# Optimization experiments

Hardware: AMD Instinct MI355X
Metric: run time of the kernel (lower is better)

Reference implementation:

```python
import jax, jax.numpy as jnp
import numpy as np

EPS_NORM = 1e-4
EPS_LOG = 1e-6


def normed_weight(W):
    # W: [O, I, K] (K=1). normalize() over dims (1,2) per output channel,
    # with norm scaled by alpha = sqrt(O / (O*I*K)) = 1/sqrt(I*K), then
    # divided again by sqrt(I*K) in get_normed_weight (eval path).
    O, I, K = W.shape
    fan_in = I * K
    norm = jnp.sqrt(jnp.sum(jnp.square(W), axis=(1, 2), keepdims=True))  # [O,1,1]
    norm = EPS_NORM + norm / np.sqrt(fan_in)
    return (W / norm) / np.sqrt(fan_in)


def complex_log(x):
    real = jnp.log(jnp.maximum(jnp.abs(x), EPS_LOG))
    imag = jnp.where(x < 0, jnp.pi, 0.0).astype(real.dtype)
    return jax.lax.complex(real, imag)


def logcumsumexp_complex(z, axis=-1):
    # stable complex logcumsumexp via associative scan:
    # logaddexp(a, b) = m + log(exp(a-m) + exp(b-m)), m = max(Re a, Re b)
    def combine(a, b):
        m = jnp.maximum(a.real, b.real)
        mc = jax.lax.complex(m, jnp.zeros_like(m))
        return mc + jnp.log(jnp.exp(a - mc) + jnp.exp(b - mc))
    return jax.lax.associative_scan(combine, z, axis=axis)


def min_gru(h, g):
    # h, g: [B, C, L]; parallel log-space minGRU recurrence along L
    log_scale = 0.5 * jnp.log(1.0 / jnp.cosh(g) + 1.0)
    log_coeffs = -jax.nn.softplus(g) + log_scale                 # real
    log_values = (-jax.nn.softplus(-g) + log_scale) + complex_log(h)  # complex
    a_star = jnp.cumsum(log_coeffs, axis=-1)                     # real
    a_star_c = jax.lax.complex(a_star, jnp.zeros_like(a_star))
    log_h = a_star_c + logcumsumexp_complex(log_values - a_star_c, axis=-1)
    return jnp.exp(log_h).real


def scaled_cat(xs, axis):
    Ns = [x.shape[axis] for x in xs]
    scale = np.sqrt(np.mean(Ns))
    return scale * jnp.concatenate([x * n ** -0.5 for n, x in zip(Ns, xs)], axis=axis)


def setup_inputs() -> dict:
    key = jax.random.key(0)
    k1, k2 = jax.random.split(key)
    B, D, L = 8, 512, 8192
    x = jax.random.normal(k1, (B, D, L), dtype=jnp.float32)
    W = jax.random.normal(k2, (2 * D, D, 1), dtype=jnp.float32)  # Conv1d(dim, 2*dim, 1) weight
    return {"x": x, "W": W}


def reference(x, W):
    Wn = normed_weight(W)  # [2D, D, 1]
    fb = jnp.einsum('oi,bil->bol', Wn[:, :, 0], x)  # [B, 2D, L]
    fore, back = jnp.split(fb, 2, axis=1)
    h_f, g_f = jnp.split(fore, 2, axis=1)
    back_r = back[..., ::-1]
    h_b, g_b = jnp.split(back_r, 2, axis=1)
    out_f = min_gru(h_f, g_f)
    out_b = min_gru(h_b, g_b)[..., ::-1]
    return scaled_cat([out_f, out_b], axis=1)
```

## Files before the change

### kernel.cpp

```cpp
#include <hip/hip_runtime.h>
#include <math.h>
#include <stdint.h>

#define LSEQ 8192
#define DIN  512
#define NB   8
#define NO   1024

typedef __bf16 bf16x8 __attribute__((ext_vector_type(8)));
typedef float f32x16 __attribute__((ext_vector_type(16)));

__device__ __forceinline__ uint32_t pack_bf16_rne(float lo, float hi) {
    uint32_t ul = __builtin_bit_cast(uint32_t, lo);
    uint32_t uh = __builtin_bit_cast(uint32_t, hi);
    ul += 0x7FFFu + ((ul >> 16) & 1u);
    uh += 0x7FFFu + ((uh >> 16) & 1u);
    return (ul >> 16) | (uh & 0xFFFF0000u);
}
__device__ __forceinline__ float bf16_lo(uint32_t w) {
    return __builtin_bit_cast(float, w << 16);
}
__device__ __forceinline__ float bf16_hi(uint32_t w) {
    return __builtin_bit_cast(float, w & 0xFFFF0000u);
}

__device__ __forceinline__ void gl_lds16(const void* g, void* l) {
    __builtin_amdgcn_global_load_lds(
        (const __attribute__((address_space(1))) void*)g,
        (__attribute__((address_space(3))) void*)l, 16, 0, 0);
}


__global__ void norm_kernel(const float* __restrict__ W, uint32_t* __restrict__ Wnb) {
    const int o = blockIdx.x;
    const int lane = threadIdx.x;
    const float* row = W + (size_t)o * DIN;
    float4 v0 = *(const float4*)(row + lane * 4);
    float4 v1 = *(const float4*)(row + 256 + lane * 4);
    float s = v0.x * v0.x + v0.y * v0.y + v0.z * v0.z + v0.w * v0.w
            + v1.x * v1.x + v1.y * v1.y + v1.z * v1.z + v1.w * v1.w;
#pragma unroll
    for (int m = 32; m; m >>= 1) s += __shfl_xor(s, m, 64);
    const float sq = 22.62741699796952f;
    const float scale = 1.0f / ((1e-4f + sqrtf(s) / sq) * sq);
    uint2 w0, w1;
    w0.x = pack_bf16_rne(v0.x * scale, v0.y * scale);
    w0.y = pack_bf16_rne(v0.z * scale, v0.w * scale);
    w1.x = pack_bf16_rne(v1.x * scale, v1.y * scale);
    w1.y = pack_bf16_rne(v1.z * scale, v1.w * scale);
    const int ot = o >> 7, mb = (o >> 5) & 3, m31 = o & 31;
    const int it0 = lane >> 3;
    const int q   = (lane >> 1) & 3;
    const int wic = (lane & 1) * 2;
    uint32_t* base = Wnb + (size_t)ot * 32768 + ((mb * 4 + q) * 32 + m31) * 4 + wic;
    *(uint2*)&base[(size_t)it0 * 2048] = w0;
    *(uint2*)&base[(size_t)(it0 + 8) * 2048] = w1;
}

__global__ __launch_bounds__(256)
void xpack_kernel(const float* __restrict__ x, uint32_t* __restrict__ xp) {
    __shared__ uint32_t sT[32 * 132];
    const int t  = threadIdx.x;
    const int bx = blockIdx.x;
    const int b  = blockIdx.y;
    const int lt = bx >> 3;
    const int ch = bx & 7;

    const float* xb = x + (size_t)b * DIN * LSEQ + lt * 128;
#pragma unroll
    for (int j = 0; j < 4; ++j) {
        const int idx = j * 256 + t;
        const int k2l = idx >> 5;
        const int lg  = idx & 31;
        const float* r0 = xb + (size_t)(2 * (ch * 32 + k2l)) * LSEQ + lg * 4;
        float4 a = *(const float4*)r0;
        float4 c = *(const float4*)(r0 + LSEQ);
        uint4 wv;
        wv.x = pack_bf16_rne(a.x, c.x);
        wv.y = pack_bf16_rne(a.y, c.y);
        wv.z = pack_bf16_rne(a.z, c.z);
        wv.w = pack_bf16_rne(a.w, c.w);
        *(uint4*)&sT[k2l * 132 + lg * 4] = wv;
    }
    __syncthreads();
    uint32_t* ob = xp + (size_t)(b * 64 + lt) * 32768;
#pragma unroll
    for (int j = 0; j < 4; ++j) {
        const int idx = j * 256 + t;
        const int lp  = idx >> 3;
        const int gq  = idx & 7;
        uint4 wv;
        wv.x = sT[(gq * 4 + 0) * 132 + lp];
        wv.y = sT[(gq * 4 + 1) * 132 + lp];
        wv.z = sT[(gq * 4 + 2) * 132 + lp];
        wv.w = sT[(gq * 4 + 3) * 132 + lp];
        const int itl   = ch * 2 + (gq >> 2);
        const int q     = gq & 3;
        const int chunk = ((lp >> 5) * 4 + q) * 32 + (lp & 31);
        *(uint4*)&ob[(size_t)itl * 2048 + chunk * 4] = wv;
    }
}

__global__ __launch_bounds__(256)
void gemm_kernel(const uint32_t* __restrict__ Wnb, const uint32_t* __restrict__ xp,
                 uint32_t* __restrict__ fbp) {
    __shared__ uint32_t sA[2][2048];
    __shared__ uint32_t sB[2][2048];

    const int tid  = threadIdx.x;
    const int lane = tid & 63;
    const int w    = tid >> 6;
    const int wm   = w & 1, wn = w >> 1;

    const int bx  = blockIdx.x;
    const int xcd = bx & 7;
    const int t   = bx >> 3;
    const int o0t = t & 7;
    const int o0  = o0t * 128;
    const int ltg = xcd + ((t >> 3) << 3);
    const int l0  = ltg * 128;
    const int b   = blockIdx.y;

    const uint32_t* gA = Wnb + (size_t)o0t * 32768 + (w * 2) * 256 + lane * 4;
    const uint32_t* gB = xp + (size_t)(b * 64 + ltg) * 32768 + (w * 2) * 256 + lane * 4;

    f32x16 acc[2][2];
#pragma unroll
    for (int i = 0; i < 2; ++i)
#pragma unroll
        for (int j = 0; j < 2; ++j)
#pragma unroll
            for (int r = 0; r < 16; ++r) acc[i][j][r] = 0.f;

#define STAGE(it, bs)                                               \
    do {                                                            \
        gl_lds16(gA + (size_t)(it) * 2048, &sA[bs][w * 512]);       \
        gl_lds16(gA + (size_t)(it) * 2048 + 256, &sA[bs][w * 512 + 256]); \
        gl_lds16(gB + (size_t)(it) * 2048, &sB[bs][w * 512]);       \
        gl_lds16(gB + (size_t)(it) * 2048 + 256, &sB[bs][w * 512 + 256]); \
    } while (0)

    STAGE(0, 0);
#pragma unroll 2
    for (int it = 0; it < 16; ++it) {
        const int cb = it & 1;
        __syncthreads();
        if (it + 1 < 16) STAGE(it + 1, cb ^ 1);
        const uint32_t* cA = sA[cb];
        const uint32_t* cB = sB[cb];
#pragma unroll
        for (int kh = 0; kh < 2; ++kh) {
            bf16x8 af[2], bfr[2];
#pragma unroll
            for (int ms = 0; ms < 2; ++ms)
                af[ms] = *(const bf16x8*)&cA[((wm * 2 + ms) * 4 + kh * 2) * 128 + lane * 4];
#pragma unroll
            for (int ns = 0; ns < 2; ++ns)
                bfr[ns] = *(const bf16x8*)&cB[((wn * 2 + ns) * 4 + kh * 2) * 128 + lane * 4];
#pragma unroll
            for (int ms = 0; ms < 2; ++ms)
#pragma unroll
                for (int ns = 0; ns < 2; ++ns)
                    acc[ms][ns] = __builtin_amdgcn_mfma_f32_32x32x16_bf16(
                        af[ms], bfr[ns], acc[ms][ns], 0, 0, 0);
        }
    }
#undef STAGE

    uint32_t* fbp_b = fbp + (size_t)b * 512 * LSEQ + l0;
#pragma unroll
    for (int ms = 0; ms < 2; ++ms)
#pragma unroll
        for (int ns = 0; ns < 2; ++ns) {
            const f32x16 a = acc[ms][ns];
            const int rb = o0 + wm * 64 + ms * 32 + 4 * (lane >> 5);
            const int cc = wn * 64 + ns * 32 + (lane & 31);
#pragma unroll
            for (int rp = 0; rp < 8; ++rp) {
                const int r = rp * 2;
                const int row = rb + (r & 3) + 8 * (r >> 2);
                fbp_b[(size_t)(row >> 1) * LSEQ + cc] = pack_bf16_rne(a[r], a[r + 1]);
            }
        }
}

__global__ __launch_bounds__(1024)
void scan_kernel(const uint32_t* __restrict__ fbp, float* __restrict__ out) {
    __shared__ float sA0[16], sB0[16], sA1[16], sB1[16];

    const int bx  = blockIdx.x;
    const int b   = blockIdx.y;
    const int dir = bx >> 7;
    const int p   = bx & 127;
    const int o2h = dir * 256 + p;
    const int o2g = dir * 256 + 128 + p;

    const int t    = threadIdx.x;
    const int lane = t & 63;
    const int w    = t >> 6;

    const uint32_t* hp = fbp + ((size_t)b * 512 + o2h) * LSEQ + t * 8;
    const uint32_t* gp = fbp + ((size_t)b * 512 + o2g) * LSEQ + t * 8;
    const uint4 h4a = *(const uint4*)(hp);
    const uint4 h4b = *(const uint4*)(hp + 4);
    const uint4 g4a = *(const uint4*)(gp);
    const uint4 g4b = *(const uint4*)(gp + 4);

    float av0[8], vv0[8], av1[8], vv1[8];
    {
        const uint32_t hws[8] = {h4a.x, h4a.y, h4a.z, h4a.w, h4b.x, h4b.y, h4b.z, h4b.w};
        const uint32_t gws[8] = {g4a.x, g4a.y, g4a.z, g4a.w, g4b.x, g4b.y, g4b.z, g4b.w};
#pragma unroll
        for (int s = 0; s < 8; ++s) {
            {
                float g_ = fminf(fmaxf(bf16_lo(gws[s]), -30.f), 30.f);
                float eg = __expf(g_);
                float a  = rsqrtf(fmaf(eg, eg, 1.f));
                float h_ = bf16_lo(hws[s]);
                av0[s] = a;
                vv0[s] = a * eg * copysignf(fmaxf(fabsf(h_), 1e-6f), h_);
            }
            {
                float g_ = fminf(fmaxf(bf16_hi(gws[s]), -30.f), 30.f);
                float eg = __expf(g_);
                float a  = rsqrtf(fmaf(eg, eg, 1.f));
                float h_ = bf16_hi(hws[s]);
                av1[s] = a;
                vv1[s] = a * eg * copysignf(fmaxf(fabsf(h_), 1e-6f), h_);
            }
        }
    }

    float A0 = 1.f, B0 = 0.f, A1 = 1.f, B1 = 0.f;
    if (dir == 0) {
#pragma unroll
        for (int i = 0; i < 8; ++i) {
            B0 = fmaf(av0[i], B0, vv0[i]); A0 *= av0[i];
            B1 = fmaf(av1[i], B1, vv1[i]); A1 *= av1[i];
        }
    } else {
#pragma unroll
        for (int i = 7; i >= 0; --i) {
            B0 = fmaf(av0[i], B0, vv0[i]); A0 *= av0[i];
            B1 = fmaf(av1[i], B1, vv1[i]); A1 *= av1[i];
        }
    }

    if (dir == 0) {
#pragma unroll
        for (int off = 1; off < 64; off <<= 1) {
            float Ap0 = __shfl_up(A0, (unsigned)off, 64), Bp0 = __shfl_up(B0, (unsigned)off, 64);
            float Ap1 = __shfl_up(A1, (unsigned)off, 64), Bp1 = __shfl_up(B1, (unsigned)off, 64);
            if (lane >= off) {
                B0 = fmaf(A0, Bp0, B0); A0 *= Ap0;
                B1 = fmaf(A1, Bp1, B1); A1 *= Ap1;
            }
        }
        if (lane == 63) { sA0[w] = A0; sB0[w] = B0; sA1[w] = A1; sB1[w] = B1; }
    } else {
#pragma unroll
        for (int off = 1; off < 64; off <<= 1) {
            float Ap0 = __shfl_down(A0, (unsigned)off, 64), Bp0 = __shfl_down(B0, (unsigned)off, 64);
            float Ap1 = __shfl_down(A1, (unsigned)off, 64), Bp1 = __shfl_down(B1, (unsigned)off, 64);
            if (lane + off < 64) {
                B0 = fmaf(A0, Bp0, B0); A0 *= Ap0;
                B1 = fmaf(A1, Bp1, B1); A1 *= Ap1;
            }
        }
        if (lane == 0) { sA0[w] = A0; sB0[w] = B0; sA1[w] = A1; sB1[w] = B1; }
    }
    __syncthreads();

    float WB0 = 0.f, WB1 = 0.f;
    if (dir == 0) {
        for (int wv = 0; wv < w; ++wv) {
            WB0 = fmaf(sA0[wv], WB0, sB0[wv]);
            WB1 = fmaf(sA1[wv], WB1, sB1[wv]);
        }
    } else {
        for (int wv = 15; wv > w; --wv) {
            WB0 = fmaf(sA0[wv], WB0, sB0[wv]);
            WB1 = fmaf(sA1[wv], WB1, sB1[wv]);
        }
    }
    float eA0, eB0, eA1, eB1;
    if (dir == 0) {
        eA0 = __shfl_up(A0, 1u, 64); eB0 = __shfl_up(B0, 1u, 64);
        eA1 = __shfl_up(A1, 1u, 64); eB1 = __shfl_up(B1, 1u, 64);
        if (lane == 0) { eA0 = 1.f; eB0 = 0.f; eA1 = 1.f; eB1 = 0.f; }
    } else {
        eA0 = __shfl_down(A0, 1u, 64); eB0 = __shfl_down(B0, 1u, 64);
        eA1 = __shfl_down(A1, 1u, 64); eB1 = __shfl_down(B1, 1u, 64);
        if (lane == 63) { eA0 = 1.f; eB0 = 0.f; eA1 = 1.f; eB1 = 0.f; }
    }
    float H0 = fmaf(eA0, WB0, eB0);
    float H1 = fmaf(eA1, WB1, eB1);

    if (dir == 0) {
#pragma unroll
        for (int i = 0; i < 8; ++i) {
            H0 = fmaf(av0[i], H0, vv0[i]); vv0[i] = H0;
            H1 = fmaf(av1[i], H1, vv1[i]); vv1[i] = H1;
        }
    } else {
#pragma unroll
        for (int i = 7; i >= 0; --i) {
            H0 = fmaf(av0[i], H0, vv0[i]); vv0[i] = H0;
            H1 = fmaf(av1[i], H1, vv1[i]); vv1[i] = H1;
        }
    }

    float* orow0 = out + ((size_t)b * 512 + dir * 256 + 2 * p) * LSEQ + t * 8;
    float* orow1 = orow0 + LSEQ;
    *(float4*)(orow0)     = make_float4(vv0[0], vv0[1], vv0[2], vv0[3]);
    *(float4*)(orow0 + 4) = make_float4(vv0[4], vv0[5], vv0[6], vv0[7]);
    *(float4*)(orow1)     = make_float4(vv1[0], vv1[1], vv1[2], vv1[3]);
    *(float4*)(orow1 + 4) = make_float4(vv1[4], vv1[5], vv1[6], vv1[7]);
}

extern "C" void kernel_launch(void* const* d_in, const int* in_sizes, int n_in,
                              void* d_out, int out_size, void* d_ws, size_t ws_size,
                              hipStream_t stream) {
    const float* x = (const float*)d_in[0];
    const float* W = (const float*)d_in[1];
    float* out = (float*)d_out;

    uint32_t* Wnb = (uint32_t*)d_ws;
    uint32_t* fbp = (uint32_t*)((char*)d_ws + (size_t)NO * DIN * 2);
    uint32_t* xp  = (uint32_t*)((char*)d_ws + (size_t)NO * DIN * 2
                                + (size_t)NB * 512 * LSEQ * 4);

    norm_kernel<<<dim3(NO), dim3(64), 0, stream>>>(W, Wnb);
    xpack_kernel<<<dim3(512, NB), dim3(256), 0, stream>>>(x, xp);
    gemm_kernel<<<dim3(512, NB), dim3(256), 0, stream>>>(Wnb, xp, fbp);
    scan_kernel<<<dim3(256, NB), dim3(1024), 0, stream>>>(fbp, out);
}
```

Before: 356.3 us.

## Process batch in two halves to shrink intermediates; swizzle xpack LDS; use native bf16 convert

The xpack, gemm and scan pipeline now runs in two passes of four batches each, so the bf16 intermediate buffers (xp and fbp) are half the size and are more likely to stay resident in the large last-level cache between kernels. The xpack transpose in shared memory gets an XOR swizzle to cut bank conflicts on the column-wise reads. The bf16 packing helper uses the compiler's native float-to-bf16 conversion instead of manual round-to-nearest-even bit arithmetic. In exchange there are more kernel launches and smaller grids per launch, which may lower occupancy in each pass.

Result: slower. 365.7 us (+2.6%).

```diff
diff --git a/kernel.cpp b/kernel.cpp
--- a/kernel.cpp
+++ b/kernel.cpp
@@ -5,17 +5,16 @@
 #define LSEQ 8192
 #define DIN  512
 #define NB   8
+#define NBH  4
 #define NO   1024
 
 typedef __bf16 bf16x8 __attribute__((ext_vector_type(8)));
 typedef float f32x16 __attribute__((ext_vector_type(16)));
 
 __device__ __forceinline__ uint32_t pack_bf16_rne(float lo, float hi) {
-    uint32_t ul = __builtin_bit_cast(uint32_t, lo);
-    uint32_t uh = __builtin_bit_cast(uint32_t, hi);
-    ul += 0x7FFFu + ((ul >> 16) & 1u);
-    uh += 0x7FFFu + ((uh >> 16) & 1u);
-    return (ul >> 16) | (uh & 0xFFFF0000u);
+    uint16_t l = __builtin_bit_cast(uint16_t, (__bf16)lo);
+    uint16_t h = __builtin_bit_cast(uint16_t, (__bf16)hi);
+    return (uint32_t)l | ((uint32_t)h << 16);
 }
 __device__ __forceinline__ float bf16_lo(uint32_t w) {
     return __builtin_bit_cast(float, w << 16);
@@ -58,11 +57,12 @@
 }
 
 __global__ __launch_bounds__(256)
-void xpack_kernel(const float* __restrict__ x, uint32_t* __restrict__ xp) {
+void xpack_kernel(const float* __restrict__ x, uint32_t* __restrict__ xp, int b0) {
     __shared__ uint32_t sT[32 * 132];
     const int t  = threadIdx.x;
     const int bx = blockIdx.x;
-    const int b  = blockIdx.y;
+    const int by = blockIdx.y;
+    const int b  = b0 + by;
     const int lt = bx >> 3;
     const int ch = bx & 7;
 
@@ -80,20 +80,22 @@
         wv.y = pack_bf16_rne(a.y, c.y);
         wv.z = pack_bf16_rne(a.z, c.z);
         wv.w = pack_bf16_rne(a.w, c.w);
-        *(uint4*)&sT[k2l * 132 + lg * 4] = wv;
+        const int sc = lg ^ (k2l >> 2);
+        *(uint4*)&sT[k2l * 132 + sc * 4] = wv;
     }
     __syncthreads();
-    uint32_t* ob = xp + (size_t)(b * 64 + lt) * 32768;
+    uint32_t* ob = xp + (size_t)(by * 64 + lt) * 32768;
 #pragma unroll
     for (int j = 0; j < 4; ++j) {
         const int idx = j * 256 + t;
         const int lp  = idx >> 3;
         const int gq  = idx & 7;
+        const int cb_ = (((lp >> 2) ^ gq) << 2) + (lp & 3);
         uint4 wv;
-        wv.x = sT[(gq * 4 + 0) * 132 + lp];
-        wv.y = sT[(gq * 4 + 1) * 132 + lp];
-        wv.z = sT[(gq * 4 + 2) * 132 + lp];
-        wv.w = sT[(gq * 4 + 3) * 132 + lp];
+        wv.x = sT[(gq * 4 + 0) * 132 + cb_];
+        wv.y = sT[(gq * 4 + 1) * 132 + cb_];
+        wv.z = sT[(gq * 4 + 2) * 132 + cb_];
+        wv.w = sT[(gq * 4 + 3) * 132 + cb_];
         const int itl   = ch * 2 + (gq >> 2);
         const int q     = gq & 3;
         const int chunk = ((lp >> 5) * 4 + q) * 32 + (lp & 31);
@@ -119,10 +121,10 @@
     const int o0  = o0t * 128;
     const int ltg = xcd + ((t >> 3) << 3);
     const int l0  = ltg * 128;
-    const int b   = blockIdx.y;
+    const int by  = blockIdx.y;
 
     const uint32_t* gA = Wnb + (size_t)o0t * 32768 + (w * 2) * 256 + lane * 4;
-    const uint32_t* gB = xp + (size_t)(b * 64 + ltg) * 32768 + (w * 2) * 256 + lane * 4;
+    const uint32_t* gB = xp + (size_t)(by * 64 + ltg) * 32768 + (w * 2) * 256 + lane * 4;
 
     f32x16 acc[2][2];
 #pragma unroll
@@ -167,7 +169,7 @@
     }
 #undef STAGE
 
-    uint32_t* fbp_b = fbp + (size_t)b * 512 * LSEQ + l0;
+    uint32_t* fbp_b = fbp + (size_t)by * 512 * LSEQ + l0;
 #pragma unroll
     for (int ms = 0; ms < 2; ++ms)
 #pragma unroll
@@ -185,11 +187,12 @@
 }
 
 __global__ __launch_bounds__(1024)
-void scan_kernel(const uint32_t* __restrict__ fbp, float* __restrict__ out) {
+void scan_kernel(const uint32_t* __restrict__ fbp, float* __restrict__ out, int b0) {
     __shared__ float sA0[16], sB0[16], sA1[16], sB1[16];
 
     const int bx  = blockIdx.x;
-    const int b   = blockIdx.y;
+    const int by  = blockIdx.y;
+    const int b   = b0 + by;
     const int dir = bx >> 7;
     const int p   = bx & 127;
     const int o2h = dir * 256 + p;
@@ -199,8 +202,8 @@
     const int lane = t & 63;
     const int w    = t >> 6;
 
-    const uint32_t* hp = fbp + ((size_t)b * 512 + o2h) * LSEQ + t * 8;
-    const uint32_t* gp = fbp + ((size_t)b * 512 + o2g) * LSEQ + t * 8;
+    const uint32_t* hp = fbp + ((size_t)by * 512 + o2h) * LSEQ + t * 8;
+    const uint32_t* gp = fbp + ((size_t)by * 512 + o2g) * LSEQ + t * 8;
     const uint4 h4a = *(const uint4*)(hp);
     const uint4 h4b = *(const uint4*)(hp + 4);
     const uint4 g4a = *(const uint4*)(gp);
@@ -328,10 +331,12 @@
     uint32_t* Wnb = (uint32_t*)d_ws;
     uint32_t* fbp = (uint32_t*)((char*)d_ws + (size_t)NO * DIN * 2);
     uint32_t* xp  = (uint32_t*)((char*)d_ws + (size_t)NO * DIN * 2
-                                + (size_t)NB * 512 * LSEQ * 4);
+                                + (size_t)NBH * 512 * LSEQ * 4);
 
     norm_kernel<<<dim3(NO), dim3(64), 0, stream>>>(W, Wnb);
-    xpack_kernel<<<dim3(512, NB), dim3(256), 0, stream>>>(x, xp);
-    gemm_kernel<<<dim3(512, NB), dim3(256), 0, stream>>>(Wnb, xp, fbp);
-    scan_kernel<<<dim3(256, NB), dim3(1024), 0, stream>>>(fbp, out);
-}
+    for (int h = 0; h < 2; ++h) {
+        xpack_kernel<<<dim3(512, NBH), dim3(256), 0, stream>>>(x, xp, h * NBH);
+        gemm_kernel<<<dim3(512, NBH), dim3(256), 0, stream>>>(Wnb, xp, fbp);
+        scan_kernel<<<dim3(256, NBH), dim3(1024), 0, stream>>>(fbp, out, h * NBH);
+    }
+}
```
